# Optimization experiments

Hardware: AMD Instinct MI355X
Metric: run time of the kernel (lower is better)

## Reference

```python
import jax, jax.numpy as jnp
import numpy as np

MAX_BITS = 64
HIDDEN = 256
EPS = 1e-5
TEMPERATURE = 1.0  # buffer default


def _layernorm(x, gamma, beta):
    mu = jnp.mean(x, axis=-1, keepdims=True)
    var = jnp.var(x, axis=-1, keepdims=True)
    return (x - mu) * jax.lax.rsqrt(var + EPS) * gamma + beta


def setup_inputs() -> dict:
    key = jax.random.key(0)
    ks = jax.random.split(key, 8)
    B = 32768
    # binary-ish inputs in [0,1)
    a_bits = (jax.random.uniform(ks[0], (B, MAX_BITS)) < 0.5).astype(jnp.float32)
    shift_bits = (jax.random.uniform(ks[1], (B, MAX_BITS)) < 0.5).astype(jnp.float32)
    # decoder: Linear(64,256) -> LN -> ReLU -> Linear(256,256) -> LN -> ReLU -> Linear(256,64)
    def lin(k, out_d, in_d):
        bound = 1.0 / np.sqrt(in_d)
        kw, kb = jax.random.split(k)
        W = jax.random.uniform(kw, (out_d, in_d), minval=-bound, maxval=bound)
        b = jax.random.uniform(kb, (out_d,), minval=-bound, maxval=bound)
        return W, b
    W1, b1 = lin(ks[2], HIDDEN, MAX_BITS)
    W2, b2 = lin(ks[3], HIDDEN, HIDDEN)
    W3, b3 = lin(ks[4], MAX_BITS, HIDDEN)
    g1 = jnp.ones((HIDDEN,)); be1 = jnp.zeros((HIDDEN,))
    g2 = jnp.ones((HIDDEN,)); be2 = jnp.zeros((HIDDEN,))
    return {
        "a_bits": a_bits, "shift_bits": shift_bits,
        "W1": W1, "b1": b1, "g1": g1, "be1": be1,
        "W2": W2, "b2": b2, "g2": g2, "be2": be2,
        "W3": W3, "b3": b3,
    }


def reference(a_bits, shift_bits, W1, b1, g1, be1, W2, b2, g2, be2, W3, b3):
    bits = a_bits.shape[1]
    # 2-layer MLP decoder
    h = jax.nn.relu(_layernorm(shift_bits @ W1.T + b1, g1, be1))
    h = jax.nn.relu(_layernorm(h @ W2.T + b2, g2, be2))
    shift_logits = (h @ W3.T + b3)[:, :bits]
    # training path: softmax over shift positions
    shift_probs = jax.nn.softmax(shift_logits / TEMPERATURE, axis=-1)
    # Toeplitz shift-sum: out[b,i] = sum_{s<=i} probs[b,s] * a_bits[b,i-s]
    i = jnp.arange(bits)[:, None]
    s = jnp.arange(bits)[None, :]
    idx = i - s                       # [bits, bits]
    mask = (idx >= 0)
    gath = a_bits[:, jnp.where(mask, idx, 0)] * mask.astype(a_bits.dtype)  # [B, bits, bits]
    return jnp.einsum('bis,bs->bi', gath, shift_probs)
```

## Files before the change

kernel.cpp:

```cpp
#include <hip/hip_runtime.h>
#include <hip/hip_fp16.h>


typedef short s8v __attribute__((ext_vector_type(8)));
typedef float f4v __attribute__((ext_vector_type(4)));

#define HPAD 264
#define PPAD 68

#define OFF_W1F 0
#define OFF_W2F 16384
#define OFF_W3F 81920
#define OFF_B1  98304
#define OFF_G1  98560
#define OFF_BE1 98816
#define OFF_B2  99072
#define OFF_G2  99328
#define OFF_BE2 99584
#define OFF_B3  99840

__device__ __forceinline__ float b2f(unsigned short u) {
    union { unsigned int i; float f; } v; v.i = ((unsigned int)u) << 16; return v.f;
}
__device__ __forceinline__ unsigned short f2b(float f) {
    union { float f; unsigned int i; } v; v.f = f;
    return (unsigned short)((v.i + 0x7fffu + ((v.i >> 16) & 1u)) >> 16);
}
__device__ __forceinline__ unsigned int cvtpk(float a, float b) {
    unsigned int r;
    asm("v_cvt_pk_bf16_f32 %0, %1, %2" : "=v"(r) : "v"(a), "v"(b));
    return r;
}
__device__ __forceinline__ int h2i(__half2 h) { union { __half2 h; int i; } u; u.h = h; return u.i; }
__device__ __forceinline__ __half2 i2h(int i) { union { __half2 h; int i; } u; u.i = i; return u.h; }

__device__ __forceinline__ bool probe_bf16(const void* a_bits) {
    unsigned int wv = ((const unsigned int*)a_bits)[threadIdx.x & 63];
    return __ballot((wv & 0xffffu) == 0x3f80u) != 0ULL;
}

__global__ __launch_bounds__(256) void convert_kernel(
    const void* __restrict__ a_probe,
    const void* __restrict__ W1, const void* __restrict__ W2, const void* __restrict__ W3,
    const void* __restrict__ b1, const void* __restrict__ g1, const void* __restrict__ be1,
    const void* __restrict__ b2, const void* __restrict__ g2, const void* __restrict__ be2,
    const void* __restrict__ b3,
    unsigned short* __restrict__ ws)
{
    const bool isbf = probe_bf16(a_probe);
    const int t = blockIdx.x * 256 + threadIdx.x;

    if (t < 12288) {
        const void* W; int K, idx, dstbase;
        if (t < 2048)       { idx = t;         W = W1; K = 64;  dstbase = OFF_W1F + idx * 8; }
        else if (t < 10240) { idx = t - 2048;  W = W2; K = 256; dstbase = OFF_W2F + idx * 8; }
        else                { idx = t - 10240; W = W3; K = 256; dstbase = OFF_W3F + idx * 8; }
        int nt, kc, lane;
        if (t < 2048) { nt = idx >> 7; kc = (idx >> 6) & 1; lane = idx & 63; }
        else          { nt = idx >> 9; kc = (idx >> 6) & 7; lane = idx & 63; }
        const int row = nt * 16 + (lane & 15);
        const int col = kc * 32 + (lane >> 4) * 8;
        const int src = row * K + col;
        s8v o;
        if (isbf) {
            o = *(const s8v*)((const unsigned short*)W + src);
        } else {
            const float* f = (const float*)W + src;
#pragma unroll
            for (int j = 0; j < 8; ++j) o[j] = (short)f2b(f[j]);
        }
        *(s8v*)(ws + dstbase) = o;
    } else if (t < 12488) {
        const int v = t - 12288;
        const void* srcp; int base, off;
        if (v < 32)       { srcp = b1;  base = OFF_B1;  off = v * 8; }
        else if (v < 64)  { srcp = g1;  base = OFF_G1;  off = (v - 32) * 8; }
        else if (v < 96)  { srcp = be1; base = OFF_BE1; off = (v - 64) * 8; }
        else if (v < 128) { srcp = b2;  base = OFF_B2;  off = (v - 96) * 8; }
        else if (v < 160) { srcp = g2;  base = OFF_G2;  off = (v - 128) * 8; }
        else if (v < 192) { srcp = be2; base = OFF_BE2; off = (v - 160) * 8; }
        else              { srcp = b3;  base = OFF_B3;  off = (v - 192) * 8; }
#pragma unroll
        for (int j = 0; j < 8; ++j)
            ws[base + off + j] = isbf ? ((const unsigned short*)srcp)[off + j]
                                      : f2b(((const float*)srcp)[off + j]);
    }
}

template<bool BF16>
__device__ __forceinline__ float loadS(const void* p, int idx) {
    if constexpr (BF16) return b2f(((const unsigned short*)p)[idx]);
    else return ((const float*)p)[idx];
}
template<bool BF16>
__device__ __forceinline__ s8v loadA8(const void* p, int idx) {
    if constexpr (BF16) {
        return *(const s8v*)((const unsigned short*)p + idx);
    } else {
        const float* f = (const float*)p + idx;
        f4v a = *(const f4v*)f;
        f4v b = *(const f4v*)(f + 4);
        union { s8v s; unsigned int u[4]; } r;
        r.u[0] = cvtpk(a[0], a[1]);
        r.u[1] = cvtpk(a[2], a[3]);
        r.u[2] = cvtpk(b[0], b[1]);
        r.u[3] = cvtpk(b[2], b[3]);
        return r.s;
    }
}
template<bool BF16>
__device__ __forceinline__ void storeO(void* p, int idx, float v) {
    if constexpr (BF16) ((unsigned short*)p)[idx] = f2b(v);
    else ((float*)p)[idx] = v;
}

template<bool BF16>
__device__ __forceinline__ void pipeline(
    const void* a_bits, const void* shifts, const unsigned short* ws, void* out,
    short* Hs, float* Ps, float* SS)
{
    const int tid = threadIdx.x;
    const int h = tid >> 6;
    const int l = tid & 63;
    const int q = l >> 4;
    const int c = l & 15;
    const int ntb = h << 3;
    const int grow0 = (int)blockIdx.x << 4;
    const int row = q * 4;

    f4v acc1[8];
#pragma unroll
    for (int i = 0; i < 8; ++i) acc1[i] = (f4v){0.f, 0.f, 0.f, 0.f};

    const s8v xa0 = loadA8<BF16>(shifts, (grow0 + c) * 64 + q * 8);
    const s8v xa1 = loadA8<BF16>(shifts, (grow0 + c) * 64 + 32 + q * 8);
#pragma unroll
    for (int i = 0; i < 8; ++i) {
        const int nt = ntb + i;
        s8v wb0 = *(const s8v*)(ws + OFF_W1F + ((nt * 2 + 0) * 64 + l) * 8);
        s8v wb1 = *(const s8v*)(ws + OFF_W1F + ((nt * 2 + 1) * 64 + l) * 8);
        acc1[i] = __builtin_amdgcn_mfma_f32_16x16x32_bf16(xa0, wb0, acc1[i], 0, 0, 0);
        acc1[i] = __builtin_amdgcn_mfma_f32_16x16x32_bf16(xa1, wb1, acc1[i], 0, 0, 0);
    }
    {
        float s[4] = {0, 0, 0, 0}, ss[4] = {0, 0, 0, 0};
#pragma unroll
        for (int i = 0; i < 8; ++i) {
            float bias = b2f(ws[OFF_B1 + (ntb + i) * 16 + c]);
#pragma unroll
            for (int r = 0; r < 4; ++r) {
                float v = acc1[i][r] + bias;
                acc1[i][r] = v;
                s[r] += v; ss[r] += v * v;
            }
        }
#pragma unroll
        for (int m = 1; m <= 8; m <<= 1)
#pragma unroll
            for (int r = 0; r < 4; ++r) {
                s[r]  += __shfl_xor(s[r],  m, 64);
                ss[r] += __shfl_xor(ss[r], m, 64);
            }
        if (c == 0)
#pragma unroll
            for (int r = 0; r < 4; ++r) {
                SS[(h * 16 + row + r) * 2 + 0] = s[r];
                SS[(h * 16 + row + r) * 2 + 1] = ss[r];
            }
        __syncthreads();
#pragma unroll
        for (int r = 0; r < 4; ++r) {
            float st = SS[(0 * 16 + row + r) * 2 + 0] + SS[(1 * 16 + row + r) * 2 + 0];
            float sq = SS[(0 * 16 + row + r) * 2 + 1] + SS[(1 * 16 + row + r) * 2 + 1];
            float mean = st * (1.0f / 256.0f);
            float var  = fmaxf(sq * (1.0f / 256.0f) - mean * mean, 0.0f);
            s[r] = mean; ss[r] = rsqrtf(var + 1e-5f);
        }
#pragma unroll
        for (int i = 0; i < 8; ++i) {
            const int nt = ntb + i;
            float gg = b2f(ws[OFF_G1 + nt * 16 + c]);
            float bb = b2f(ws[OFF_BE1 + nt * 16 + c]);
            float y[4];
#pragma unroll
            for (int r = 0; r < 4; ++r)
                y[r] = fmaxf((acc1[i][r] - s[r]) * ss[r] * gg + bb, 0.0f);
            unsigned int u01 = cvtpk(y[0], y[1]);
            unsigned int u23 = cvtpk(y[2], y[3]);
            Hs[(row + 0) * HPAD + nt * 16 + c] = (short)(u01 & 0xffffu);
            Hs[(row + 1) * HPAD + nt * 16 + c] = (short)(u01 >> 16);
            Hs[(row + 2) * HPAD + nt * 16 + c] = (short)(u23 & 0xffffu);
            Hs[(row + 3) * HPAD + nt * 16 + c] = (short)(u23 >> 16);
        }
    }
    __syncthreads();

    f4v acc2[8];
#pragma unroll
    for (int i = 0; i < 8; ++i) acc2[i] = (f4v){0.f, 0.f, 0.f, 0.f};
#pragma unroll
    for (int ks = 0; ks < 8; ++ks) {
        s8v af = *(const s8v*)&Hs[c * HPAD + ks * 32 + q * 8];
#pragma unroll
        for (int i = 0; i < 8; ++i) {
            const int nt = ntb + i;
            s8v bf_ = *(const s8v*)(ws + OFF_W2F + ((nt * 8 + ks) * 64 + l) * 8);
            acc2[i] = __builtin_amdgcn_mfma_f32_16x16x32_bf16(af, bf_, acc2[i], 0, 0, 0);
        }
    }
    {
        float s[4] = {0, 0, 0, 0}, ss[4] = {0, 0, 0, 0};
#pragma unroll
        for (int i = 0; i < 8; ++i) {
            float bias = b2f(ws[OFF_B2 + (ntb + i) * 16 + c]);
#pragma unroll
            for (int r = 0; r < 4; ++r) {
                float v = acc2[i][r] + bias;
                acc2[i][r] = v;
                s[r] += v; ss[r] += v * v;
            }
        }
#pragma unroll
        for (int m = 1; m <= 8; m <<= 1)
#pragma unroll
            for (int r = 0; r < 4; ++r) {
                s[r]  += __shfl_xor(s[r],  m, 64);
                ss[r] += __shfl_xor(ss[r], m, 64);
            }
        if (c == 0)
#pragma unroll
            for (int r = 0; r < 4; ++r) {
                SS[(h * 16 + row + r) * 2 + 0] = s[r];
                SS[(h * 16 + row + r) * 2 + 1] = ss[r];
            }
        __syncthreads();
#pragma unroll
        for (int r = 0; r < 4; ++r) {
            float st = SS[(0 * 16 + row + r) * 2 + 0] + SS[(1 * 16 + row + r) * 2 + 0];
            float sq = SS[(0 * 16 + row + r) * 2 + 1] + SS[(1 * 16 + row + r) * 2 + 1];
            float mean = st * (1.0f / 256.0f);
            float var  = fmaxf(sq * (1.0f / 256.0f) - mean * mean, 0.0f);
            s[r] = mean; ss[r] = rsqrtf(var + 1e-5f);
        }
#pragma unroll
        for (int i = 0; i < 8; ++i) {
            const int nt = ntb + i;
            float gg = b2f(ws[OFF_G2 + nt * 16 + c]);
            float bb = b2f(ws[OFF_BE2 + nt * 16 + c]);
            float y[4];
#pragma unroll
            for (int r = 0; r < 4; ++r)
                y[r] = fmaxf((acc2[i][r] - s[r]) * ss[r] * gg + bb, 0.0f);
            unsigned int u01 = cvtpk(y[0], y[1]);
            unsigned int u23 = cvtpk(y[2], y[3]);
            Hs[(row + 0) * HPAD + nt * 16 + c] = (short)(u01 & 0xffffu);
            Hs[(row + 1) * HPAD + nt * 16 + c] = (short)(u01 >> 16);
            Hs[(row + 2) * HPAD + nt * 16 + c] = (short)(u23 & 0xffffu);
            Hs[(row + 3) * HPAD + nt * 16 + c] = (short)(u23 >> 16);
        }
    }
    __syncthreads();

    f4v acc3[2];
#pragma unroll
    for (int t = 0; t < 2; ++t) acc3[t] = (f4v){0.f, 0.f, 0.f, 0.f};
#pragma unroll
    for (int ks = 0; ks < 8; ++ks) {
        s8v af = *(const s8v*)&Hs[c * HPAD + ks * 32 + q * 8];
#pragma unroll
        for (int t = 0; t < 2; ++t) {
            const int nt = h * 2 + t;
            s8v bf_ = *(const s8v*)(ws + OFF_W3F + ((nt * 8 + ks) * 64 + l) * 8);
            acc3[t] = __builtin_amdgcn_mfma_f32_16x16x32_bf16(af, bf_, acc3[t], 0, 0, 0);
        }
    }
    {
        float sum[4] = {0, 0, 0, 0};
#pragma unroll
        for (int t = 0; t < 2; ++t) {
            const int nt = h * 2 + t;
            const float bias = b2f(ws[OFF_B3 + nt * 16 + c]);
#pragma unroll
            for (int r = 0; r < 4; ++r) {
                float e = __expf(acc3[t][r] + bias);
                Ps[(row + r) * PPAD + nt * 16 + c] = e;
                sum[r] += e;
            }
        }
#pragma unroll
        for (int m = 1; m <= 8; m <<= 1)
#pragma unroll
            for (int r = 0; r < 4; ++r)
                sum[r] += __shfl_xor(sum[r], m, 64);
        if (c == 0)
#pragma unroll
            for (int r = 0; r < 4; ++r)
                SS[(h * 16 + row + r) * 2 + 1] = sum[r];
    }
    __syncthreads();

#pragma unroll
    for (int jj = 0; jj < 4; ++jj) {
        const int j = h * 4 + jj;
        const int m0 = j, m1 = j + 8;
        float S0 = SS[(0 * 16 + m0) * 2 + 1] + SS[(1 * 16 + m0) * 2 + 1];
        float S1 = SS[(0 * 16 + m1) * 2 + 1] + SS[(1 * 16 + m1) * 2 + 1];
        const float i0 = __builtin_amdgcn_rcpf(S0);
        const float i1 = __builtin_amdgcn_rcpf(S1);
        __half2 pph = __floats2half2_rn(Ps[m0 * PPAD + l] * i0,
                                        Ps[m1 * PPAD + l] * i1);
        const int ppi = h2i(pph);
        __half2 aah = __floats2half2_rn(loadS<BF16>(a_bits, (grow0 + m0) * 64 + l),
                                        loadS<BF16>(a_bits, (grow0 + m1) * 64 + l));
        int rr = h2i(aah);
        __half2 acc = __float2half2_rn(0.0f);
#pragma unroll
        for (int s = 0; s < 64; ++s) {
            const int spi = __builtin_amdgcn_readlane(ppi, s);
            acc = __hfma2(i2h(spi), i2h(rr), acc);
            if (s < 63)
                rr = __builtin_amdgcn_update_dpp(0, rr, 0x138, 0xF, 0xF, true);
        }
        storeO<BF16>(out, (grow0 + m0) * 64 + l, __low2float(acc));
        storeO<BF16>(out, (grow0 + m1) * 64 + l, __high2float(acc));
    }
}

__global__ __launch_bounds__(128, 4) void shiftdec_kernel(
    const void* __restrict__ a_bits, const void* __restrict__ shifts,
    const unsigned short* __restrict__ ws, void* __restrict__ out)
{
    __shared__ __align__(16) short Hs[16 * HPAD];
    __shared__ __align__(16) float Ps[16 * PPAD];
    __shared__ __align__(16) float SSb[2 * 16 * 2];

    if (probe_bf16(a_bits))
        pipeline<true>(a_bits, shifts, ws, out, Hs, Ps, SSb);
    else
        pipeline<false>(a_bits, shifts, ws, out, Hs, Ps, SSb);
}

extern "C" void kernel_launch(void* const* d_in, const int* in_sizes, int n_in,
                              void* d_out, int out_size, void* d_ws, size_t ws_size,
                              hipStream_t stream) {
    const int B = in_sizes[0] / 64;
    const int grid = B / 16;

    hipLaunchKernelGGL(convert_kernel, dim3(49), dim3(256), 0, stream,
                       d_in[0], d_in[2], d_in[6], d_in[10],
                       d_in[3], d_in[4], d_in[5], d_in[7], d_in[8], d_in[9], d_in[11],
                       (unsigned short*)d_ws);
    hipLaunchKernelGGL(shiftdec_kernel, dim3(grid), dim3(128), 0, stream,
                       d_in[0], d_in[1], (const unsigned short*)d_ws, d_out);
}
```

Baseline: 112.5 us.

## Process 32 rows per block with 4 waves splitting N, reusing weight fragments

Each block now handles 32 batch rows with 256 threads. Every wave owns a quarter of the hidden columns and covers two 16-row M tiles, so each loaded weight fragment feeds two MFMAs. This halves per-row weight traffic from global/L2. The cost is more shared memory per block, a 4-way LayerNorm partial reduction through a wider stats buffer, and half as many blocks.

```diff
diff --git a/kernel.cpp b/kernel.cpp
--- a/kernel.cpp
+++ b/kernel.cpp
@@ -114,199 +114,179 @@
     else ((float*)p)[idx] = v;
 }
 
+__device__ __forceinline__ void ln_relu_store(
+    f4v* acc, const unsigned short* ws, int offB, int offG, int offBe,
+    short* Hs, float* SS, int w, int q, int c, int row, int ntb)
+{
+    float sm[2][4], sv[2][4];
+#pragma unroll
+    for (int mt = 0; mt < 2; ++mt)
+#pragma unroll
+        for (int r = 0; r < 4; ++r) { sm[mt][r] = 0.f; sv[mt][r] = 0.f; }
+#pragma unroll
+    for (int i = 0; i < 4; ++i) {
+        const float bias = b2f(ws[offB + (ntb + i) * 16 + c]);
+#pragma unroll
+        for (int mt = 0; mt < 2; ++mt)
+#pragma unroll
+            for (int r = 0; r < 4; ++r) {
+                float v = acc[mt * 4 + i][r] + bias;
+                acc[mt * 4 + i][r] = v;
+                sm[mt][r] += v; sv[mt][r] += v * v;
+            }
+    }
+#pragma unroll
+    for (int m = 1; m <= 8; m <<= 1)
+#pragma unroll
+        for (int mt = 0; mt < 2; ++mt)
+#pragma unroll
+            for (int r = 0; r < 4; ++r) {
+                sm[mt][r] += __shfl_xor(sm[mt][r], m, 64);
+                sv[mt][r] += __shfl_xor(sv[mt][r], m, 64);
+            }
+    if (c == 0)
+#pragma unroll
+        for (int mt = 0; mt < 2; ++mt)
+#pragma unroll
+            for (int r = 0; r < 4; ++r) {
+                const int g = mt * 16 + row + r;
+                *(float2*)&SS[g * 8 + w * 2] = make_float2(sm[mt][r], sv[mt][r]);
+            }
+    __syncthreads();
+#pragma unroll
+    for (int mt = 0; mt < 2; ++mt)
+#pragma unroll
+        for (int r = 0; r < 4; ++r) {
+            const int g = mt * 16 + row + r;
+            f4v v0 = *(const f4v*)&SS[g * 8];
+            f4v v1 = *(const f4v*)&SS[g * 8 + 4];
+            float st = v0[0] + v0[2] + v1[0] + v1[2];
+            float sq = v0[1] + v0[3] + v1[1] + v1[3];
+            float mean = st * (1.0f / 256.0f);
+            float var  = fmaxf(sq * (1.0f / 256.0f) - mean * mean, 0.0f);
+            sm[mt][r] = mean; sv[mt][r] = rsqrtf(var + 1e-5f);
+        }
+#pragma unroll
+    for (int i = 0; i < 4; ++i) {
+        const int nt = ntb + i;
+        const float gg = b2f(ws[offG + nt * 16 + c]);
+        const float bb = b2f(ws[offBe + nt * 16 + c]);
+#pragma unroll
+        for (int mt = 0; mt < 2; ++mt) {
+            float y[4];
+#pragma unroll
+            for (int r = 0; r < 4; ++r)
+                y[r] = fmaxf((acc[mt * 4 + i][r] - sm[mt][r]) * sv[mt][r] * gg + bb, 0.0f);
+            unsigned int u01 = cvtpk(y[0], y[1]);
+            unsigned int u23 = cvtpk(y[2], y[3]);
+            Hs[(mt * 16 + row + 0) * HPAD + nt * 16 + c] = (short)(u01 & 0xffffu);
+            Hs[(mt * 16 + row + 1) * HPAD + nt * 16 + c] = (short)(u01 >> 16);
+            Hs[(mt * 16 + row + 2) * HPAD + nt * 16 + c] = (short)(u23 & 0xffffu);
+            Hs[(mt * 16 + row + 3) * HPAD + nt * 16 + c] = (short)(u23 >> 16);
+        }
+    }
+}
+
 template<bool BF16>
 __device__ __forceinline__ void pipeline(
     const void* a_bits, const void* shifts, const unsigned short* ws, void* out,
     short* Hs, float* Ps, float* SS)
 {
     const int tid = threadIdx.x;
-    const int h = tid >> 6;
+    const int w = tid >> 6;
     const int l = tid & 63;
     const int q = l >> 4;
     const int c = l & 15;
-    const int ntb = h << 3;
-    const int grow0 = (int)blockIdx.x << 4;
+    const int ntb = w << 2;
+    const int grow0 = (int)blockIdx.x << 5;
     const int row = q * 4;
 
     f4v acc1[8];
 #pragma unroll
     for (int i = 0; i < 8; ++i) acc1[i] = (f4v){0.f, 0.f, 0.f, 0.f};
 
-    const s8v xa0 = loadA8<BF16>(shifts, (grow0 + c) * 64 + q * 8);
-    const s8v xa1 = loadA8<BF16>(shifts, (grow0 + c) * 64 + 32 + q * 8);
-#pragma unroll
-    for (int i = 0; i < 8; ++i) {
+    const s8v xa00 = loadA8<BF16>(shifts, (grow0 + c) * 64 + q * 8);
+    const s8v xa01 = loadA8<BF16>(shifts, (grow0 + c) * 64 + 32 + q * 8);
+    const s8v xa10 = loadA8<BF16>(shifts, (grow0 + 16 + c) * 64 + q * 8);
+    const s8v xa11 = loadA8<BF16>(shifts, (grow0 + 16 + c) * 64 + 32 + q * 8);
+#pragma unroll
+    for (int i = 0; i < 4; ++i) {
         const int nt = ntb + i;
         s8v wb0 = *(const s8v*)(ws + OFF_W1F + ((nt * 2 + 0) * 64 + l) * 8);
         s8v wb1 = *(const s8v*)(ws + OFF_W1F + ((nt * 2 + 1) * 64 + l) * 8);
-        acc1[i] = __builtin_amdgcn_mfma_f32_16x16x32_bf16(xa0, wb0, acc1[i], 0, 0, 0);
-        acc1[i] = __builtin_amdgcn_mfma_f32_16x16x32_bf16(xa1, wb1, acc1[i], 0, 0, 0);
+        acc1[i]     = __builtin_amdgcn_mfma_f32_16x16x32_bf16(xa00, wb0, acc1[i], 0, 0, 0);
+        acc1[i]     = __builtin_amdgcn_mfma_f32_16x16x32_bf16(xa01, wb1, acc1[i], 0, 0, 0);
+        acc1[4 + i] = __builtin_amdgcn_mfma_f32_16x16x32_bf16(xa10, wb0, acc1[4 + i], 0, 0, 0);
+        acc1[4 + i] = __builtin_amdgcn_mfma_f32_16x16x32_bf16(xa11, wb1, acc1[4 + i], 0, 0, 0);
+    }
+    ln_relu_store(acc1, ws, OFF_B1, OFF_G1, OFF_BE1, Hs, SS, w, q, c, row, ntb);
+    __syncthreads();
+
+    f4v acc2[8];
+#pragma unroll
+    for (int i = 0; i < 8; ++i) acc2[i] = (f4v){0.f, 0.f, 0.f, 0.f};
+#pragma unroll
+    for (int ks = 0; ks < 8; ++ks) {
+        s8v af0 = *(const s8v*)&Hs[c * HPAD + ks * 32 + q * 8];
+        s8v af1 = *(const s8v*)&Hs[(16 + c) * HPAD + ks * 32 + q * 8];
+#pragma unroll
+        for (int i = 0; i < 4; ++i) {
+            s8v bf_ = *(const s8v*)(ws + OFF_W2F + (((ntb + i) * 8 + ks) * 64 + l) * 8);
+            acc2[i]     = __builtin_amdgcn_mfma_f32_16x16x32_bf16(af0, bf_, acc2[i], 0, 0, 0);
+            acc2[4 + i] = __builtin_amdgcn_mfma_f32_16x16x32_bf16(af1, bf_, acc2[4 + i], 0, 0, 0);
+        }
+    }
+    ln_relu_store(acc2, ws, OFF_B2, OFF_G2, OFF_BE2, Hs, SS, w, q, c, row, ntb);
+    __syncthreads();
+
+    f4v acc3[2];
+#pragma unroll
+    for (int t = 0; t < 2; ++t) acc3[t] = (f4v){0.f, 0.f, 0.f, 0.f};
+#pragma unroll
+    for (int ks = 0; ks < 8; ++ks) {
+        s8v af0 = *(const s8v*)&Hs[c * HPAD + ks * 32 + q * 8];
+        s8v af1 = *(const s8v*)&Hs[(16 + c) * HPAD + ks * 32 + q * 8];
+        s8v bf_ = *(const s8v*)(ws + OFF_W3F + ((w * 8 + ks) * 64 + l) * 8);
+        acc3[0] = __builtin_amdgcn_mfma_f32_16x16x32_bf16(af0, bf_, acc3[0], 0, 0, 0);
+        acc3[1] = __builtin_amdgcn_mfma_f32_16x16x32_bf16(af1, bf_, acc3[1], 0, 0, 0);
     }
     {
-        float s[4] = {0, 0, 0, 0}, ss[4] = {0, 0, 0, 0};
-#pragma unroll
-        for (int i = 0; i < 8; ++i) {
-            float bias = b2f(ws[OFF_B1 + (ntb + i) * 16 + c]);
+        const float bias = b2f(ws[OFF_B3 + w * 16 + c]);
+        float sum[2][4];
+#pragma unroll
+        for (int mt = 0; mt < 2; ++mt)
 #pragma unroll
             for (int r = 0; r < 4; ++r) {
-                float v = acc1[i][r] + bias;
-                acc1[i][r] = v;
-                s[r] += v; ss[r] += v * v;
+                float e = __expf(acc3[mt][r] + bias);
+                Ps[(mt * 16 + row + r) * PPAD + w * 16 + c] = e;
+                sum[mt][r] = e;
             }
-        }
 #pragma unroll
         for (int m = 1; m <= 8; m <<= 1)
 #pragma unroll
-            for (int r = 0; r < 4; ++r) {
-                s[r]  += __shfl_xor(s[r],  m, 64);
-                ss[r] += __shfl_xor(ss[r], m, 64);
-            }
+            for (int mt = 0; mt < 2; ++mt)
+#pragma unroll
+                for (int r = 0; r < 4; ++r)
+                    sum[mt][r] += __shfl_xor(sum[mt][r], m, 64);
         if (c == 0)
 #pragma unroll
-            for (int r = 0; r < 4; ++r) {
-                SS[(h * 16 + row + r) * 2 + 0] = s[r];
-                SS[(h * 16 + row + r) * 2 + 1] = ss[r];
-            }
-        __syncthreads();
-#pragma unroll
-        for (int r = 0; r < 4; ++r) {
-            float st = SS[(0 * 16 + row + r) * 2 + 0] + SS[(1 * 16 + row + r) * 2 + 0];
-            float sq = SS[(0 * 16 + row + r) * 2 + 1] + SS[(1 * 16 + row + r) * 2 + 1];
-            float mean = st * (1.0f / 256.0f);
-            float var  = fmaxf(sq * (1.0f / 256.0f) - mean * mean, 0.0f);
-            s[r] = mean; ss[r] = rsqrtf(var + 1e-5f);
-        }
-#pragma unroll
-        for (int i = 0; i < 8; ++i) {
-            const int nt = ntb + i;
-            float gg = b2f(ws[OFF_G1 + nt * 16 + c]);
-            float bb = b2f(ws[OFF_BE1 + nt * 16 + c]);
-            float y[4];
-#pragma unroll
-            for (int r = 0; r < 4; ++r)
-                y[r] = fmaxf((acc1[i][r] - s[r]) * ss[r] * gg + bb, 0.0f);
-            unsigned int u01 = cvtpk(y[0], y[1]);
-            unsigned int u23 = cvtpk(y[2], y[3]);
-            Hs[(row + 0) * HPAD + nt * 16 + c] = (short)(u01 & 0xffffu);
-            Hs[(row + 1) * HPAD + nt * 16 + c] = (short)(u01 >> 16);
-            Hs[(row + 2) * HPAD + nt * 16 + c] = (short)(u23 & 0xffffu);
-            Hs[(row + 3) * HPAD + nt * 16 + c] = (short)(u23 >> 16);
-        }
+            for (int mt = 0; mt < 2; ++mt)
+#pragma unroll
+                for (int r = 0; r < 4; ++r)
+                    SS[(mt * 16 + row + r) * 8 + w * 2 + 1] = sum[mt][r];
     }
     __syncthreads();
 
-    f4v acc2[8];
-#pragma unroll
-    for (int i = 0; i < 8; ++i) acc2[i] = (f4v){0.f, 0.f, 0.f, 0.f};
-#pragma unroll
-    for (int ks = 0; ks < 8; ++ks) {
-        s8v af = *(const s8v*)&Hs[c * HPAD + ks * 32 + q * 8];
-#pragma unroll
-        for (int i = 0; i < 8; ++i) {
-            const int nt = ntb + i;
-            s8v bf_ = *(const s8v*)(ws + OFF_W2F + ((nt * 8 + ks) * 64 + l) * 8);
-            acc2[i] = __builtin_amdgcn_mfma_f32_16x16x32_bf16(af, bf_, acc2[i], 0, 0, 0);
-        }
-    }
-    {
-        float s[4] = {0, 0, 0, 0}, ss[4] = {0, 0, 0, 0};
-#pragma unroll
-        for (int i = 0; i < 8; ++i) {
-            float bias = b2f(ws[OFF_B2 + (ntb + i) * 16 + c]);
-#pragma unroll
-            for (int r = 0; r < 4; ++r) {
-                float v = acc2[i][r] + bias;
-                acc2[i][r] = v;
-                s[r] += v; ss[r] += v * v;
-            }
-        }
-#pragma unroll
-        for (int m = 1; m <= 8; m <<= 1)
-#pragma unroll
-            for (int r = 0; r < 4; ++r) {
-                s[r]  += __shfl_xor(s[r],  m, 64);
-                ss[r] += __shfl_xor(ss[r], m, 64);
-            }
-        if (c == 0)
-#pragma unroll
-            for (int r = 0; r < 4; ++r) {
-                SS[(h * 16 + row + r) * 2 + 0] = s[r];
-                SS[(h * 16 + row + r) * 2 + 1] = ss[r];
-            }
-        __syncthreads();
-#pragma unroll
-        for (int r = 0; r < 4; ++r) {
-            float st = SS[(0 * 16 + row + r) * 2 + 0] + SS[(1 * 16 + row + r) * 2 + 0];
-            float sq = SS[(0 * 16 + row + r) * 2 + 1] + SS[(1 * 16 + row + r) * 2 + 1];
-            float mean = st * (1.0f / 256.0f);
-            float var  = fmaxf(sq * (1.0f / 256.0f) - mean * mean, 0.0f);
-            s[r] = mean; ss[r] = rsqrtf(var + 1e-5f);
-        }
-#pragma unroll
-        for (int i = 0; i < 8; ++i) {
-            const int nt = ntb + i;
-            float gg = b2f(ws[OFF_G2 + nt * 16 + c]);
-            float bb = b2f(ws[OFF_BE2 + nt * 16 + c]);
-            float y[4];
-#pragma unroll
-            for (int r = 0; r < 4; ++r)
-                y[r] = fmaxf((acc2[i][r] - s[r]) * ss[r] * gg + bb, 0.0f);
-            unsigned int u01 = cvtpk(y[0], y[1]);
-            unsigned int u23 = cvtpk(y[2], y[3]);
-            Hs[(row + 0) * HPAD + nt * 16 + c] = (short)(u01 & 0xffffu);
-            Hs[(row + 1) * HPAD + nt * 16 + c] = (short)(u01 >> 16);
-            Hs[(row + 2) * HPAD + nt * 16 + c] = (short)(u23 & 0xffffu);
-            Hs[(row + 3) * HPAD + nt * 16 + c] = (short)(u23 >> 16);
-        }
-    }
-    __syncthreads();
-
-    f4v acc3[2];
-#pragma unroll
-    for (int t = 0; t < 2; ++t) acc3[t] = (f4v){0.f, 0.f, 0.f, 0.f};
-#pragma unroll
-    for (int ks = 0; ks < 8; ++ks) {
-        s8v af = *(const s8v*)&Hs[c * HPAD + ks * 32 + q * 8];
-#pragma unroll
-        for (int t = 0; t < 2; ++t) {
-            const int nt = h * 2 + t;
-            s8v bf_ = *(const s8v*)(ws + OFF_W3F + ((nt * 8 + ks) * 64 + l) * 8);
-            acc3[t] = __builtin_amdgcn_mfma_f32_16x16x32_bf16(af, bf_, acc3[t], 0, 0, 0);
-        }
-    }
-    {
-        float sum[4] = {0, 0, 0, 0};
-#pragma unroll
-        for (int t = 0; t < 2; ++t) {
-            const int nt = h * 2 + t;
-            const float bias = b2f(ws[OFF_B3 + nt * 16 + c]);
-#pragma unroll
-            for (int r = 0; r < 4; ++r) {
-                float e = __expf(acc3[t][r] + bias);
-                Ps[(row + r) * PPAD + nt * 16 + c] = e;
-                sum[r] += e;
-            }
-        }
-#pragma unroll
-        for (int m = 1; m <= 8; m <<= 1)
-#pragma unroll
-            for (int r = 0; r < 4; ++r)
-                sum[r] += __shfl_xor(sum[r], m, 64);
-        if (c == 0)
-#pragma unroll
-            for (int r = 0; r < 4; ++r)
-                SS[(h * 16 + row + r) * 2 + 1] = sum[r];
-    }
-    __syncthreads();
-
 #pragma unroll
     for (int jj = 0; jj < 4; ++jj) {
-        const int j = h * 4 + jj;
-        const int m0 = j, m1 = j + 8;
-        float S0 = SS[(0 * 16 + m0) * 2 + 1] + SS[(1 * 16 + m0) * 2 + 1];
-        float S1 = SS[(0 * 16 + m1) * 2 + 1] + SS[(1 * 16 + m1) * 2 + 1];
-        const float i0 = __builtin_amdgcn_rcpf(S0);
-        const float i1 = __builtin_amdgcn_rcpf(S1);
+        const int m0 = w * 8 + jj;
+        const int m1 = m0 + 4;
+        f4v u0 = *(const f4v*)&SS[m0 * 8];
+        f4v u1 = *(const f4v*)&SS[m0 * 8 + 4];
+        f4v u2 = *(const f4v*)&SS[m1 * 8];
+        f4v u3 = *(const f4v*)&SS[m1 * 8 + 4];
+        const float i0 = __builtin_amdgcn_rcpf(u0[1] + u0[3] + u1[1] + u1[3]);
+        const float i1 = __builtin_amdgcn_rcpf(u2[1] + u2[3] + u3[1] + u3[3]);
         __half2 pph = __floats2half2_rn(Ps[m0 * PPAD + l] * i0,
                                         Ps[m1 * PPAD + l] * i1);
         const int ppi = h2i(pph);
@@ -326,13 +306,13 @@
     }
 }
 
-__global__ __launch_bounds__(128, 4) void shiftdec_kernel(
+__global__ __launch_bounds__(256, 4) void shiftdec_kernel(
     const void* __restrict__ a_bits, const void* __restrict__ shifts,
     const unsigned short* __restrict__ ws, void* __restrict__ out)
 {
-    __shared__ __align__(16) short Hs[16 * HPAD];
-    __shared__ __align__(16) float Ps[16 * PPAD];
-    __shared__ __align__(16) float SSb[2 * 16 * 2];
+    __shared__ __align__(16) short Hs[32 * HPAD];
+    __shared__ __align__(16) float Ps[32 * PPAD];
+    __shared__ __align__(16) float SSb[32 * 8];
 
     if (probe_bf16(a_bits))
         pipeline<true>(a_bits, shifts, ws, out, Hs, Ps, SSb);
@@ -344,12 +324,12 @@
                               void* d_out, int out_size, void* d_ws, size_t ws_size,
                               hipStream_t stream) {
     const int B = in_sizes[0] / 64;
-    const int grid = B / 16;
+    const int grid = B / 32;
 
     hipLaunchKernelGGL(convert_kernel, dim3(49), dim3(256), 0, stream,
                        d_in[0], d_in[2], d_in[6], d_in[10],
                        d_in[3], d_in[4], d_in[5], d_in[7], d_in[8], d_in[9], d_in[11],
                        (unsigned short*)d_ws);
-    hipLaunchKernelGGL(shiftdec_kernel, dim3(grid), dim3(128), 0, stream,
+    hipLaunchKernelGGL(shiftdec_kernel, dim3(grid), dim3(256), 0, stream,
                        d_in[0], d_in[1], (const unsigned short*)d_ws, d_out);
 }
```

New measurement: 108.3 us, median of 2. 1.04x faster.
